# Optimization experiments

Hardware: AMD Instinct MI355X
Metric: run time of the kernel (lower is better)

Reference implementation:

```python
import jax, jax.numpy as jnp
import numpy as np

N_EMBD = 1024
HEAD_SIZE = N_EMBD  # source bug: Block passes n_embd as head_size
EPS = 1e-5

def layernorm(x, g, b):
    mu = jnp.mean(x, axis=-1, keepdims=True)
    var = jnp.var(x, axis=-1, keepdims=True)
    return (x - mu) * jax.lax.rsqrt(var + EPS) * g + b

def setup_inputs() -> dict:
    key = jax.random.key(0)
    ks = jax.random.split(key, 8)
    B, T, C = 4, 2048, N_EMBD
    s = lambda fan_in: 1.0 / np.sqrt(fan_in)
    return {
        "x": jax.random.normal(ks[0], (B, T, C), dtype=jnp.float32),
        "Wk": jax.random.uniform(ks[1], (C, HEAD_SIZE), jnp.float32, -s(C), s(C)),
        "Wq": jax.random.uniform(ks[2], (C, HEAD_SIZE), jnp.float32, -s(C), s(C)),
        "Wv": jax.random.uniform(ks[3], (C, HEAD_SIZE), jnp.float32, -s(C), s(C)),
        "W1": jax.random.uniform(ks[4], (C, 4 * C), jnp.float32, -s(C), s(C)),
        "b1": jnp.zeros((4 * C,), jnp.float32),
        "W2": jax.random.uniform(ks[5], (4 * C, C), jnp.float32, -s(4 * C), s(4 * C)),
        "b2": jnp.zeros((C,), jnp.float32),
        "g1": jnp.ones((C,), jnp.float32),
        "be1": jnp.zeros((C,), jnp.float32),
        "g2": jnp.ones((C,), jnp.float32),
        "be2": jnp.zeros((C,), jnp.float32),
    }

def reference(x, Wk, Wq, Wv, W1, b1, W2, b2, g1, be1, g2, be2):
    B, T, C = x.shape
    h = layernorm(x, g1, be1)
    q = h @ Wq              # [B,T,H]
    k = h @ Wk
    v = h @ Wv
    wei = jnp.einsum('bth,bsh->bts', q, k) / jnp.sqrt(jnp.float32(C))
    causal = jnp.tril(jnp.ones((T, T), dtype=bool))
    wei = jnp.where(causal, wei, -jnp.inf)
    wei = jax.nn.softmax(wei, axis=-1)
    sa = jnp.einsum('bts,bsh->bth', wei, v)
    x = x + sa
    h2 = layernorm(x, g2, be2)
    ff = jax.nn.relu(h2 @ W1 + b1) @ W2 + b2
    return x + ff
```

## Files before the change

kernel.cpp:

```cpp
#include <hip/hip_runtime.h>
#include <hip/hip_bf16.h>


typedef __bf16 bf16x8_t __attribute__((ext_vector_type(8)));
typedef float f32x4_t __attribute__((ext_vector_type(4)));

__device__ __forceinline__ unsigned short f2bf(float f) {
    unsigned int u = __float_as_uint(f);
    u += 0x7fffu + ((u >> 16) & 1u);
    return (unsigned short)(u >> 16);
}

__device__ __forceinline__ void gload16(const void* g, void* lds) {
    __builtin_amdgcn_global_load_lds(
        (const __attribute__((address_space(1))) unsigned int*)g,
        (__attribute__((address_space(3))) unsigned int*)lds, 16, 0, 0);
}

enum { EPI_F32 = 0, EPI_BF16 = 1, EPI_BIAS_RELU_BF16 = 2, EPI_RESID_F32 = 3,
       EPI_BIAS_RESID_F32 = 4 };

template <int EPI, bool CSKIP, bool KLIM>
__global__ __launch_bounds__(256, 3) void gemm_k(
    const unsigned short* __restrict__ A,
    const unsigned short* __restrict__ B,
    void* __restrict__ Cout,
    const float* __restrict__ bias,
    const float* __restrict__ resid,
    int M, int N, int K, int lda, int ldb, float scale,
    long long batA, long long batB, long long batC, long long batR)
{
    constexpr int BM = 128, BN = 128, BK = 32;
    __shared__ __align__(16) unsigned short sA[BM * BK];
    __shared__ __align__(16) unsigned short sB[BN * BK];

    const int row0 = blockIdx.y * BM;
    const int col0 = blockIdx.x * BN;
    if (CSKIP && col0 > row0) return;

    const int bz = blockIdx.z;
    const unsigned short* Ab = A + (long long)bz * batA + (long long)row0 * lda;
    const unsigned short* Bb = B + (long long)bz * batB + (long long)col0 * ldb;

    const int tid  = threadIdx.x;
    const int lane = tid & 63;
    const int wid  = tid >> 6;
    const int wr   = (wid >> 1) * 64;
    const int wc   = (wid & 1) * 64;
    const int lr   = lane & 15;
    const int lg   = lane >> 4;

    int Keff = K;
    if (KLIM) { int kl = row0 + BM; Keff = kl < K ? kl : K; }
    const int nkt = Keff / BK;

    const int c0 = wid * 64 + lane;
    const int c1 = c0 + 256;
    const unsigned short* ga0 = Ab + (long long)(c0 >> 2) * lda + (c0 & 3) * 8;
    const unsigned short* ga1 = Ab + (long long)(c1 >> 2) * lda + (c1 & 3) * 8;
    const unsigned short* gb0 = Bb + (long long)(c0 >> 2) * ldb + (c0 & 3) * 8;
    const unsigned short* gb1 = Bb + (long long)(c1 >> 2) * ldb + (c1 & 3) * 8;
    unsigned short* sAd0 = sA + (wid * 64) * 8;
    unsigned short* sAd1 = sA + (256 + wid * 64) * 8;
    unsigned short* sBd0 = sB + (wid * 64) * 8;
    unsigned short* sBd1 = sB + (256 + wid * 64) * 8;

    int aoff[4], boff[4];
#pragma unroll
    for (int m = 0; m < 4; ++m) aoff[m] = (wr + m * 16 + lr) * BK + lg * 8;
#pragma unroll
    for (int n = 0; n < 4; ++n) boff[n] = (wc + n * 16 + lr) * BK + lg * 8;

    f32x4_t acc[4][4];
#pragma unroll
    for (int m = 0; m < 4; ++m)
#pragma unroll
        for (int n = 0; n < 4; ++n)
            acc[m][n] = (f32x4_t){0.f, 0.f, 0.f, 0.f};

    for (int kt = 0; kt < nkt; ++kt) {
        __syncthreads();
        const int ke = kt * BK;
        gload16(ga0 + ke, sAd0);
        gload16(ga1 + ke, sAd1);
        gload16(gb0 + ke, sBd0);
        gload16(gb1 + ke, sBd1);
        __syncthreads();

        bf16x8_t af[4], bfv[4];
#pragma unroll
        for (int m = 0; m < 4; ++m) af[m]  = *(const bf16x8_t*)(sA + aoff[m]);
#pragma unroll
        for (int n = 0; n < 4; ++n) bfv[n] = *(const bf16x8_t*)(sB + boff[n]);
#pragma unroll
        for (int m = 0; m < 4; ++m)
#pragma unroll
            for (int n = 0; n < 4; ++n)
                acc[m][n] = __builtin_amdgcn_mfma_f32_16x16x32_bf16(
                    af[m], bfv[n], acc[m][n], 0, 0, 0);
    }

    const int ldc = N;
    float* Cf = (float*)Cout + (long long)bz * batC;
    unsigned short* Cb = (unsigned short*)Cout + (long long)bz * batC;
    const float* R = nullptr;
    if constexpr (EPI == EPI_RESID_F32 || EPI == EPI_BIAS_RESID_F32)
        R = resid + (long long)bz * batR;

#pragma unroll
    for (int m = 0; m < 4; ++m)
#pragma unroll
        for (int n = 0; n < 4; ++n)
#pragma unroll
            for (int j = 0; j < 4; ++j) {
                const int row = row0 + wr + m * 16 + lg * 4 + j;
                const int col = col0 + wc + n * 16 + lr;
                const long long idx = (long long)row * ldc + col;
                float v = acc[m][n][j] * scale;
                if constexpr (EPI == EPI_F32) {
                    Cf[idx] = v;
                } else if constexpr (EPI == EPI_BF16) {
                    Cb[idx] = f2bf(v);
                } else if constexpr (EPI == EPI_BIAS_RELU_BF16) {
                    v += bias[col];
                    v = v > 0.f ? v : 0.f;
                    Cb[idx] = f2bf(v);
                } else if constexpr (EPI == EPI_RESID_F32) {
                    Cf[idx] = v + R[idx];
                } else {
                    Cf[idx] = v + bias[col] + R[idx];
                }
            }
}

__global__ __launch_bounds__(256) void tconv_k(
    const float* __restrict__ in, unsigned short* __restrict__ out,
    int R, int Cc)
{
    __shared__ float t[64][65];
    const int r0 = blockIdx.y * 64, c0 = blockIdx.x * 64;
    const int tid = threadIdx.x;
    const int a = tid >> 4;
    const int b = tid & 15;
#pragma unroll
    for (int i = 0; i < 4; ++i) {
        const int row = a + i * 16;
        float4 v = *(const float4*)(in + (long long)(r0 + row) * Cc + c0 + b * 4);
        t[row][b * 4 + 0] = v.x; t[row][b * 4 + 1] = v.y;
        t[row][b * 4 + 2] = v.z; t[row][b * 4 + 3] = v.w;
    }
    __syncthreads();
#pragma unroll
    for (int i = 0; i < 4; ++i) {
        const int oc = a + i * 16;
        ushort4 o;
        o.x = f2bf(t[b * 4 + 0][oc]);
        o.y = f2bf(t[b * 4 + 1][oc]);
        o.z = f2bf(t[b * 4 + 2][oc]);
        o.w = f2bf(t[b * 4 + 3][oc]);
        *(ushort4*)(out + (long long)(c0 + oc) * R + r0 + b * 4) = o;
    }
}

__global__ __launch_bounds__(256) void ln_k(
    const float* __restrict__ x, const float* __restrict__ g,
    const float* __restrict__ be, unsigned short* __restrict__ out)
{
    __shared__ float sred[8];
    const long long row = blockIdx.x;
    const int tid = threadIdx.x;
    float4 v = ((const float4*)(x + row * 1024))[tid];
    float s = v.x + v.y + v.z + v.w;
    float q = v.x * v.x + v.y * v.y + v.z * v.z + v.w * v.w;
#pragma unroll
    for (int off = 32; off > 0; off >>= 1) {
        s += __shfl_xor(s, off);
        q += __shfl_xor(q, off);
    }
    if ((tid & 63) == 0) { sred[tid >> 6] = s; sred[4 + (tid >> 6)] = q; }
    __syncthreads();
    s = sred[0] + sred[1] + sred[2] + sred[3];
    q = sred[4] + sred[5] + sred[6] + sred[7];
    const float mean = s * (1.0f / 1024.0f);
    const float var  = q * (1.0f / 1024.0f) - mean * mean;
    const float rstd = rsqrtf(var + 1e-5f);
    float4 gv = ((const float4*)g)[tid];
    float4 bv = ((const float4*)be)[tid];
    ushort4 o;
    o.x = f2bf((v.x - mean) * rstd * gv.x + bv.x);
    o.y = f2bf((v.y - mean) * rstd * gv.y + bv.y);
    o.z = f2bf((v.z - mean) * rstd * gv.z + bv.z);
    o.w = f2bf((v.w - mean) * rstd * gv.w + bv.w);
    *(ushort4*)(out + row * 1024 + tid * 4) = o;
}

__global__ __launch_bounds__(256) void softmax_k(
    const float* __restrict__ S, unsigned short* __restrict__ P, int T)
{
    __shared__ float rowl[2048];
    __shared__ float sred[4];
    const int t = blockIdx.x;
    const long long base = ((long long)blockIdx.y * T + t) * (long long)T;
    const float* srow = S + base;
    unsigned short* prow = P + base;
    const int n = t + 1;
    const int lim = ((t >> 7) + 1) << 7;
    const int tid = threadIdx.x;

    const int nv = n >> 2;
    for (int i = tid; i < nv; i += 256)
        ((float4*)rowl)[i] = ((const float4*)srow)[i];
    for (int i = (nv << 2) + tid; i < n; i += 256) rowl[i] = srow[i];
    __syncthreads();

    float mx = -3.0e38f;
    for (int i = tid; i < n; i += 256) mx = fmaxf(mx, rowl[i]);
#pragma unroll
    for (int off = 32; off > 0; off >>= 1) mx = fmaxf(mx, __shfl_xor(mx, off));
    if ((tid & 63) == 0) sred[tid >> 6] = mx;
    __syncthreads();
    mx = fmaxf(fmaxf(sred[0], sred[1]), fmaxf(sred[2], sred[3]));
    __syncthreads();

    float sum = 0.f;
    for (int i = tid; i < n; i += 256) {
        float e = __expf(rowl[i] - mx);
        rowl[i] = e;
        sum += e;
    }
#pragma unroll
    for (int off = 32; off > 0; off >>= 1) sum += __shfl_xor(sum, off);
    if ((tid & 63) == 0) sred[tid >> 6] = sum;
    __syncthreads();
    sum = sred[0] + sred[1] + sred[2] + sred[3];
    const float inv = 1.0f / sum;

    for (int i = tid; i < n; i += 256) prow[i] = f2bf(rowl[i] * inv);
    for (int i = n + tid; i < lim; i += 256) prow[i] = 0;
}

extern "C" void kernel_launch(void* const* d_in, const int* in_sizes, int n_in,
                              void* d_out, int out_size, void* d_ws, size_t ws_size,
                              hipStream_t stream)
{
    const int B = 4, T = 2048, C = 1024, F = 4096;
    const float* x   = (const float*)d_in[0];
    const float* Wk  = (const float*)d_in[1];
    const float* Wq  = (const float*)d_in[2];
    const float* Wv  = (const float*)d_in[3];
    const float* W1  = (const float*)d_in[4];
    const float* b1  = (const float*)d_in[5];
    const float* W2  = (const float*)d_in[6];
    const float* b2  = (const float*)d_in[7];
    const float* g1  = (const float*)d_in[8];
    const float* be1 = (const float*)d_in[9];
    const float* g2  = (const float*)d_in[10];
    const float* be2 = (const float*)d_in[11];

    char* ws = (char*)d_ws;
    const size_t MB = 1ull << 20;
    unsigned short* h    = (unsigned short*)(ws + 0);
    unsigned short* q    = (unsigned short*)(ws + 16 * MB);
    unsigned short* k    = (unsigned short*)(ws + 32 * MB);
    unsigned short* vT   = (unsigned short*)(ws + 48 * MB);
    float*          xres = (float*)(ws + 64 * MB);
    float*          S    = (float*)(ws + 96 * MB);
    unsigned short* ff1  = (unsigned short*)(ws + 96 * MB);
    unsigned short* P    = (unsigned short*)(ws + 160 * MB);
    unsigned short* wqT  = (unsigned short*)(ws + 192 * MB);
    unsigned short* wkT  = (unsigned short*)(ws + 194 * MB);
    unsigned short* wvT  = (unsigned short*)(ws + 196 * MB);
    unsigned short* w1T  = (unsigned short*)(ws + 198 * MB);
    unsigned short* w2T  = (unsigned short*)(ws + 206 * MB);

    tconv_k<<<dim3(16, 16), 256, 0, stream>>>(Wq, wqT, C, C);
    tconv_k<<<dim3(16, 16), 256, 0, stream>>>(Wk, wkT, C, C);
    tconv_k<<<dim3(16, 16), 256, 0, stream>>>(Wv, wvT, C, C);
    tconv_k<<<dim3(64, 16), 256, 0, stream>>>(W1, w1T, C, F);
    tconv_k<<<dim3(16, 64), 256, 0, stream>>>(W2, w2T, F, C);

    ln_k<<<dim3(B * T), 256, 0, stream>>>(x, g1, be1, h);

    dim3 gqk(C / 128, (B * T) / 128, 1);
    gemm_k<EPI_BF16, false, false><<<gqk, 256, 0, stream>>>(
        h, wqT, q, nullptr, nullptr, B * T, C, C, C, C, 1.0f, 0, 0, 0, 0);
    gemm_k<EPI_BF16, false, false><<<gqk, 256, 0, stream>>>(
        h, wkT, k, nullptr, nullptr, B * T, C, C, C, C, 1.0f, 0, 0, 0, 0);

    dim3 gvt((B * T) / 128, C / 128, 1);
    gemm_k<EPI_BF16, false, false><<<gvt, 256, 0, stream>>>(
        wvT, h, vT, nullptr, nullptr, C, B * T, C, C, C, 1.0f, 0, 0, 0, 0);

    dim3 gsc(T / 128, T / 128, B);
    gemm_k<EPI_F32, true, false><<<gsc, 256, 0, stream>>>(
        q, k, S, nullptr, nullptr, T, T, C, C, C, 0.03125f,
        (long long)T * C, (long long)T * C, (long long)T * T, 0);

    softmax_k<<<dim3(T, B), 256, 0, stream>>>(S, P, T);

    dim3 gsa(C / 128, T / 128, B);
    gemm_k<EPI_RESID_F32, false, true><<<gsa, 256, 0, stream>>>(
        P, vT, xres, nullptr, x, T, C, T, T, B * T, 1.0f,
        (long long)T * T, (long long)T, (long long)T * C, (long long)T * C);

    ln_k<<<dim3(B * T), 256, 0, stream>>>(xres, g2, be2, h);

    dim3 gf1(F / 128, (B * T) / 128, 1);
    gemm_k<EPI_BIAS_RELU_BF16, false, false><<<gf1, 256, 0, stream>>>(
        h, w1T, ff1, b1, nullptr, B * T, F, C, C, C, 1.0f, 0, 0, 0, 0);

    dim3 gf2(C / 128, (B * T) / 128, 1);
    gemm_k<EPI_BIAS_RESID_F32, false, false><<<gf2, 256, 0, stream>>>(
        ff1, w2T, (float*)d_out, b2, xres, B * T, C, F, F, F, 1.0f, 0, 0, 0, 0);
}
```

Baseline: 419.1 us.

## Replace 128x128 GEMM with double-buffered 256x256 tile kernel using swizzled LDS

Replaces the single-buffered 128x128x32 GEMM with a 512-thread 256x256x64 kernel. It double-buffers LDS (128KB), prefetches the next K tile in stages, and overlaps those loads with MFMA via explicit vmcnt waits and barriers. It also XOR-swizzles the LDS layout to avoid bank conflicts, remaps workgroup order for L2 locality, and raises MFMA priority with setprio. The softmax padding limit is changed to 256 to match the new causal tile granularity. The larger tiles give fewer workgroups, which may cost occupancy on the smaller GEMMs, and the waitcnt counts rely on exact ordering of the load instructions.

Result: slower. 481.3 us (+14.8%).

```diff
diff --git a/kernel.cpp b/kernel.cpp
--- a/kernel.cpp
+++ b/kernel.cpp
@@ -21,83 +21,133 @@
        EPI_BIAS_RESID_F32 = 4 };
 
 template <int EPI, bool CSKIP, bool KLIM>
-__global__ __launch_bounds__(256, 3) void gemm_k(
+__global__ __launch_bounds__(512, 2) void gemm256(
     const unsigned short* __restrict__ A,
-    const unsigned short* __restrict__ B,
+    const unsigned short* __restrict__ Bm,
     void* __restrict__ Cout,
     const float* __restrict__ bias,
     const float* __restrict__ resid,
     int M, int N, int K, int lda, int ldb, float scale,
     long long batA, long long batB, long long batC, long long batR)
 {
-    constexpr int BM = 128, BN = 128, BK = 32;
-    __shared__ __align__(16) unsigned short sA[BM * BK];
-    __shared__ __align__(16) unsigned short sB[BN * BK];
-
-    const int row0 = blockIdx.y * BM;
-    const int col0 = blockIdx.x * BN;
+    __shared__ __align__(16) unsigned char lds[131072];
+
+    const int gx = gridDim.x;
+    const int nwg = gx * gridDim.y;
+    int bl = blockIdx.y * gx + blockIdx.x;
+    bl = (bl & 7) * (nwg >> 3) + (bl >> 3);
+    const int bx = bl % gx, by = bl / gx;
+
+    const int row0 = by * 256, col0 = bx * 256;
     if (CSKIP && col0 > row0) return;
 
     const int bz = blockIdx.z;
     const unsigned short* Ab = A + (long long)bz * batA + (long long)row0 * lda;
-    const unsigned short* Bb = B + (long long)bz * batB + (long long)col0 * ldb;
-
-    const int tid  = threadIdx.x;
-    const int lane = tid & 63;
-    const int wid  = tid >> 6;
-    const int wr   = (wid >> 1) * 64;
-    const int wc   = (wid & 1) * 64;
-    const int lr   = lane & 15;
-    const int lg   = lane >> 4;
+    const unsigned short* Bb = Bm + (long long)bz * batB + (long long)col0 * ldb;
+
+    const int tid = threadIdx.x, lane = tid & 63, wid = tid >> 6;
+    const int wrM = (wid >> 2) * 128;
+    const int wcN = (wid & 3) * 64;
+    const int lr = lane & 15, lg = lane >> 4;
 
     int Keff = K;
-    if (KLIM) { int kl = row0 + BM; Keff = kl < K ? kl : K; }
-    const int nkt = Keff / BK;
-
-    const int c0 = wid * 64 + lane;
-    const int c1 = c0 + 256;
-    const unsigned short* ga0 = Ab + (long long)(c0 >> 2) * lda + (c0 & 3) * 8;
-    const unsigned short* ga1 = Ab + (long long)(c1 >> 2) * lda + (c1 & 3) * 8;
-    const unsigned short* gb0 = Bb + (long long)(c0 >> 2) * ldb + (c0 & 3) * 8;
-    const unsigned short* gb1 = Bb + (long long)(c1 >> 2) * ldb + (c1 & 3) * 8;
-    unsigned short* sAd0 = sA + (wid * 64) * 8;
-    unsigned short* sAd1 = sA + (256 + wid * 64) * 8;
-    unsigned short* sBd0 = sB + (wid * 64) * 8;
-    unsigned short* sBd1 = sB + (256 + wid * 64) * 8;
-
-    int aoff[4], boff[4];
-#pragma unroll
-    for (int m = 0; m < 4; ++m) aoff[m] = (wr + m * 16 + lr) * BK + lg * 8;
-#pragma unroll
-    for (int n = 0; n < 4; ++n) boff[n] = (wc + n * 16 + lr) * BK + lg * 8;
-
-    f32x4_t acc[4][4];
-#pragma unroll
-    for (int m = 0; m < 4; ++m)
+    if (KLIM) { int kl = row0 + 256; Keff = kl < K ? kl : K; }
+    const int nkt = Keff >> 6;
+
+    int rowc[2], scol[2];
+#pragma unroll
+    for (int i = 0; i < 2; ++i) {
+        const int c = wid * 128 + i * 64 + lane;
+        rowc[i] = c >> 2;
+        scol[i] = (c & 3) ^ (rowc[i] & 3);
+    }
+    const unsigned short* gA[2];
+    const unsigned short* gB[2];
+#pragma unroll
+    for (int i = 0; i < 2; ++i) {
+        gA[i] = Ab + (long long)rowc[i] * lda + scol[i] * 8;
+        gB[i] = Bb + (long long)rowc[i] * ldb + scol[i] * 8;
+    }
+    const int ldsW = wid * 2048;
+
+    const int sw = (lg ^ (lr & 3)) << 4;
+    const int aoff = (wrM + lr) * 64 + sw;
+    const int boff = (wcN + lr) * 64 + sw + 16384;
+
+    f32x4_t acc[8][4];
+#pragma unroll
+    for (int m = 0; m < 8; ++m)
 #pragma unroll
         for (int n = 0; n < 4; ++n)
             acc[m][n] = (f32x4_t){0.f, 0.f, 0.f, 0.f};
 
-    for (int kt = 0; kt < nkt; ++kt) {
-        __syncthreads();
-        const int ke = kt * BK;
-        gload16(ga0 + ke, sAd0);
-        gload16(ga1 + ke, sAd1);
-        gload16(gb0 + ke, sBd0);
-        gload16(gb1 + ke, sBd1);
-        __syncthreads();
-
-        bf16x8_t af[4], bfv[4];
-#pragma unroll
-        for (int m = 0; m < 4; ++m) af[m]  = *(const bf16x8_t*)(sA + aoff[m]);
-#pragma unroll
-        for (int n = 0; n < 4; ++n) bfv[n] = *(const bf16x8_t*)(sB + boff[n]);
-#pragma unroll
-        for (int m = 0; m < 4; ++m)
-#pragma unroll
-            for (int n = 0; n < 4; ++n)
-                acc[m][n] = __builtin_amdgcn_mfma_f32_16x16x32_bf16(
-                    af[m], bfv[n], acc[m][n], 0, 0, 0);
+    auto stage = [&](int buf, int kk, int op, int kt) {
+        const int ke = kt * 64 + kk * 32;
+        const unsigned short* g0 = (op ? gB[0] : gA[0]) + ke;
+        const unsigned short* g1 = (op ? gB[1] : gA[1]) + ke;
+        unsigned char* d = lds + buf * 65536 + kk * 32768 + op * 16384 + ldsW;
+        gload16(g0, d);
+        gload16(g1, d + 1024);
+    };
+
+    bf16x8_t af[8], bv[2];
+    auto dsA = [&](int buf, int kk) {
+#pragma unroll
+        for (int m = 0; m < 8; ++m)
+            af[m] = *(const bf16x8_t*)(lds + buf * 65536 + kk * 32768 + aoff + m * 1024);
+    };
+    auto dsB = [&](int buf, int kk, int n0) {
+#pragma unroll
+        for (int j = 0; j < 2; ++j)
+            bv[j] = *(const bf16x8_t*)(lds + buf * 65536 + kk * 32768 + boff + (n0 + j) * 1024);
+    };
+    auto mfma16 = [&](int n0) {
+        __builtin_amdgcn_s_setprio(1);
+#pragma unroll
+        for (int m = 0; m < 8; ++m)
+#pragma unroll
+            for (int j = 0; j < 2; ++j)
+                acc[m][n0 + j] = __builtin_amdgcn_mfma_f32_16x16x32_bf16(
+                    af[m], bv[j], acc[m][n0 + j], 0, 0, 0);
+        __builtin_amdgcn_s_setprio(0);
+    };
+
+    stage(0, 0, 0, 0); stage(0, 0, 1, 0); stage(0, 1, 0, 0); stage(0, 1, 1, 0);
+
+    auto tile = [&](int kt, int buf) {
+        const bool pre = (kt + 1 < nkt);
+        const int nb = buf ^ 1;
+        if (pre) {
+            stage(nb, 0, 0, kt + 1);
+            asm volatile("s_waitcnt vmcnt(6)\ns_barrier" ::: "memory");
+        } else {
+            asm volatile("s_waitcnt vmcnt(4)\ns_barrier" ::: "memory");
+        }
+        dsA(buf, 0); dsB(buf, 0, 0);
+        mfma16(0);
+        asm volatile("s_barrier" ::: "memory");
+        if (pre) stage(nb, 0, 1, kt + 1);
+        dsB(buf, 0, 2);
+        mfma16(2);
+        asm volatile("s_barrier" ::: "memory");
+        if (pre) {
+            stage(nb, 1, 0, kt + 1);
+            asm volatile("s_waitcnt vmcnt(6)\ns_barrier" ::: "memory");
+        } else {
+            asm volatile("s_waitcnt vmcnt(0)\ns_barrier" ::: "memory");
+        }
+        dsA(buf, 1); dsB(buf, 1, 0);
+        mfma16(0);
+        asm volatile("s_barrier" ::: "memory");
+        if (pre) stage(nb, 1, 1, kt + 1);
+        dsB(buf, 1, 2);
+        mfma16(2);
+        asm volatile("s_barrier" ::: "memory");
+    };
+
+    for (int kt = 0; kt < nkt; kt += 2) {
+        tile(kt, 0);
+        tile(kt + 1, 1);
     }
 
     const int ldc = N;
@@ -108,13 +158,13 @@
         R = resid + (long long)bz * batR;
 
 #pragma unroll
-    for (int m = 0; m < 4; ++m)
+    for (int m = 0; m < 8; ++m)
 #pragma unroll
         for (int n = 0; n < 4; ++n)
 #pragma unroll
             for (int j = 0; j < 4; ++j) {
-                const int row = row0 + wr + m * 16 + lg * 4 + j;
-                const int col = col0 + wc + n * 16 + lr;
+                const int row = row0 + wrM + m * 16 + lg * 4 + j;
+                const int col = col0 + wcN + n * 16 + lr;
                 const long long idx = (long long)row * ldc + col;
                 float v = acc[m][n][j] * scale;
                 if constexpr (EPI == EPI_F32) {
@@ -204,7 +254,7 @@
     const float* srow = S + base;
     unsigned short* prow = P + base;
     const int n = t + 1;
-    const int lim = ((t >> 7) + 1) << 7;
+    const int lim = ((t >> 8) + 1) << 8;
     const int tid = threadIdx.x;
 
     const int nv = n >> 2;
@@ -281,35 +331,35 @@
 
     ln_k<<<dim3(B * T), 256, 0, stream>>>(x, g1, be1, h);
 
-    dim3 gqk(C / 128, (B * T) / 128, 1);
-    gemm_k<EPI_BF16, false, false><<<gqk, 256, 0, stream>>>(
+    dim3 gqk(C / 256, (B * T) / 256, 1);
+    gemm256<EPI_BF16, false, false><<<gqk, 512, 0, stream>>>(
         h, wqT, q, nullptr, nullptr, B * T, C, C, C, C, 1.0f, 0, 0, 0, 0);
-    gemm_k<EPI_BF16, false, false><<<gqk, 256, 0, stream>>>(
+    gemm256<EPI_BF16, false, false><<<gqk, 512, 0, stream>>>(
         h, wkT, k, nullptr, nullptr, B * T, C, C, C, C, 1.0f, 0, 0, 0, 0);
 
-    dim3 gvt((B * T) / 128, C / 128, 1);
-    gemm_k<EPI_BF16, false, false><<<gvt, 256, 0, stream>>>(
+    dim3 gvt((B * T) / 256, C / 256, 1);
+    gemm256<EPI_BF16, false, false><<<gvt, 512, 0, stream>>>(
         wvT, h, vT, nullptr, nullptr, C, B * T, C, C, C, 1.0f, 0, 0, 0, 0);
 
-    dim3 gsc(T / 128, T / 128, B);
-    gemm_k<EPI_F32, true, false><<<gsc, 256, 0, stream>>>(
+    dim3 gsc(T / 256, T / 256, B);
+    gemm256<EPI_F32, true, false><<<gsc, 512, 0, stream>>>(
         q, k, S, nullptr, nullptr, T, T, C, C, C, 0.03125f,
         (long long)T * C, (long long)T * C, (long long)T * T, 0);
 
     softmax_k<<<dim3(T, B), 256, 0, stream>>>(S, P, T);
 
-    dim3 gsa(C / 128, T / 128, B);
-    gemm_k<EPI_RESID_F32, false, true><<<gsa, 256, 0, stream>>>(
+    dim3 gsa(C / 256, T / 256, B);
+    gemm256<EPI_RESID_F32, false, true><<<gsa, 512, 0, stream>>>(
         P, vT, xres, nullptr, x, T, C, T, T, B * T, 1.0f,
         (long long)T * T, (long long)T, (long long)T * C, (long long)T * C);
 
     ln_k<<<dim3(B * T), 256, 0, stream>>>(xres, g2, be2, h);
 
-    dim3 gf1(F / 128, (B * T) / 128, 1);
-    gemm_k<EPI_BIAS_RELU_BF16, false, false><<<gf1, 256, 0, stream>>>(
+    dim3 gf1(F / 256, (B * T) / 256, 1);
+    gemm256<EPI_BIAS_RELU_BF16, false, false><<<gf1, 512, 0, stream>>>(
         h, w1T, ff1, b1, nullptr, B * T, F, C, C, C, 1.0f, 0, 0, 0, 0);
 
-    dim3 gf2(C / 128, (B * T) / 128, 1);
-    gemm_k<EPI_BIAS_RESID_F32, false, false><<<gf2, 256, 0, stream>>>(
+    dim3 gf2(C / 256, (B * T) / 256, 1);
+    gemm256<EPI_BIAS_RESID_F32, false, false><<<gf2, 512, 0, stream>>>(
         ff1, w2T, (float*)d_out, b2, xres, B * T, C, F, F, F, 1.0f, 0, 0, 0, 0);
 }
```
